# Performance work log

Measured on AMD Instinct MI355X. Metric: run time of the kernel, lower is better.

The kernel has to match this reference:

```python
import jax, jax.numpy as jnp
import numpy as np

EMBED_DIM = 1024
NUM_HEADS = 16
HEAD_DIM = EMBED_DIM // NUM_HEADS


def setup_inputs() -> dict:
    key = jax.random.key(0)
    ks = jax.random.split(key, 7)
    B, S, D = 8, 1024, EMBED_DIM
    scale = 1.0 / np.sqrt(D)
    x = jax.random.normal(ks[0], (B, S, D), dtype=jnp.float32)
    Wq = jax.random.normal(ks[1], (D, D), dtype=jnp.float32) * scale
    Wk = jax.random.normal(ks[2], (D, D), dtype=jnp.float32) * scale
    Wv = jax.random.normal(ks[3], (D, D), dtype=jnp.float32) * scale
    bq = jax.random.normal(ks[4], (D,), dtype=jnp.float32) * 0.01
    bk = jax.random.normal(ks[5], (D,), dtype=jnp.float32) * 0.01
    bv = jax.random.normal(ks[6], (D,), dtype=jnp.float32) * 0.01
    return {"x": x, "Wq": Wq, "Wk": Wk, "Wv": Wv, "bq": bq, "bk": bk, "bv": bv}


def reference(x, Wq, Wk, Wv, bq, bk, bv):
    B, S, D = x.shape
    H, Hd = NUM_HEADS, HEAD_DIM
    # torch nn.Linear: y = x @ W.T + b
    q = (x @ Wq.T + bq).reshape(B, S, H, Hd).transpose(0, 2, 1, 3)  # [B,H,S,Hd]
    k = (x @ Wk.T + bk).reshape(B, S, H, Hd).transpose(0, 2, 1, 3)
    v = (x @ Wv.T + bv).reshape(B, S, H, Hd).transpose(0, 2, 1, 3)
    scale = Hd ** -0.5
    scores = jnp.einsum('bhqd,bhkd->bhqk', q, k) * scale  # [B,H,S,S]
    attn = jax.nn.softmax(scores, axis=-1)
    # dropout_rate = 0.0 -> identity; out_proj is never applied in the source forward
    ctx = jnp.einsum('bhqk,bhkd->bhqd', attn, v)  # [B,H,S,Hd]
    return ctx.transpose(0, 2, 1, 3).reshape(B, S, D)
```

## Files before the change

kernel.cpp:

```cpp
#include <hip/hip_runtime.h>
#include <hip/hip_bf16.h>
#include <cstdint>
#include <cstddef>


typedef __attribute__((ext_vector_type(8))) short bf16x8;
typedef __attribute__((ext_vector_type(8))) unsigned short u16x8;
typedef __attribute__((ext_vector_type(4))) float f32x4;
typedef __attribute__((ext_vector_type(16))) float f32x16;
typedef __attribute__((ext_vector_type(4))) unsigned int u32x4;
typedef __attribute__((ext_vector_type(2))) unsigned int u32x2;

typedef const __attribute__((address_space(1))) void* gptr_t;
typedef __attribute__((address_space(3))) void* lptr_t;

#define LOG2E 1.44269504088896340736f

__device__ __forceinline__ unsigned short f2bf(float f) {
  unsigned int u = __float_as_uint(f);
  u += 0x7fffu + ((u >> 16) & 1u);
  return (unsigned short)(u >> 16);
}

__device__ __forceinline__ unsigned int pack_bf16x2(float lo, float hi) {
  const __hip_bfloat162 h = __float22bfloat162_rn(float2{lo, hi});
  unsigned int u;
  __builtin_memcpy(&u, &h, 4);
  return u;
}

__global__ void cvt_all(const float* __restrict__ x, const float* __restrict__ wq,
                        const float* __restrict__ wk, const float* __restrict__ wv,
                        unsigned short* __restrict__ Xb, unsigned short* __restrict__ Wb) {
  const int b = blockIdx.x;
  const float* src;
  unsigned short* dst;
  int i;
  if (b < 8192) {
    src = x; dst = Xb; i = b * 256 + threadIdx.x;
  } else {
    const int s = b - 8192;
    const int sel = s >> 10;
    src = (sel == 0) ? wq : (sel == 1) ? wk : wv;
    dst = Wb + (size_t)sel * 1048576;
    i = (s & 1023) * 256 + threadIdx.x;
  }
  float4 v = reinterpret_cast<const float4*>(src)[i];
  ushort4 o;
  o.x = f2bf(v.x); o.y = f2bf(v.y); o.z = f2bf(v.z); o.w = f2bf(v.w);
  reinterpret_cast<ushort4*>(dst)[i] = o;
}

__global__ __launch_bounds__(256) void qkv_gemm(
    const unsigned short* __restrict__ Xb, const unsigned short* __restrict__ Wb,
    const float* __restrict__ bq, const float* __restrict__ bk,
    const float* __restrict__ bv,
    unsigned short* __restrict__ Qo, unsigned short* __restrict__ Ko,
    unsigned short* __restrict__ Vo) {
  __shared__ unsigned short As[128 * 32];
  __shared__ unsigned short Bs[128 * 32];

  const int tid = threadIdx.x;
  const int lane = tid & 63;
  const int w = tid >> 6;
  const int wr = w >> 1, wc = w & 1;
  const int bm = blockIdx.x & 63;
  const int bn = blockIdx.x >> 6;

  const f32x4 vzero = {0.f, 0.f, 0.f, 0.f};
  f32x4 acc[4][4];
#pragma unroll
  for (int m = 0; m < 4; ++m)
#pragma unroll
    for (int n = 0; n < 4; ++n) acc[m][n] = vzero;

  const int c0 = w * 2, c1 = w * 2 + 1;
  const int srow0 = c0 * 16 + (lane >> 2);
  const int srow1 = c1 * 16 + (lane >> 2);
  const int scol = (lane & 3) * 8;
  const unsigned short* gA0 = Xb + (size_t)(bm * 128 + srow0) * 1024 + scol;
  const unsigned short* gA1 = Xb + (size_t)(bm * 128 + srow1) * 1024 + scol;
  const unsigned short* gB0 = Wb + (size_t)(bn * 128 + srow0) * 1024 + scol;
  const unsigned short* gB1 = Wb + (size_t)(bn * 128 + srow1) * 1024 + scol;
  char* lA0 = (char*)As + c0 * 1024;
  char* lA1 = (char*)As + c1 * 1024;
  char* lB0 = (char*)Bs + c0 * 1024;
  char* lB1 = (char*)Bs + c1 * 1024;

  const int aoff = (wr * 64 + (lane & 15)) * 64 + (lane >> 4) * 16;
  const int boff = (wc * 64 + (lane & 15)) * 64 + (lane >> 4) * 16;

  for (int kt = 0; kt < 32; ++kt) {
    const int k0 = kt * 32;
    __builtin_amdgcn_global_load_lds((gptr_t)(gA0 + k0), (lptr_t)lA0, 16, 0, 0);
    __builtin_amdgcn_global_load_lds((gptr_t)(gA1 + k0), (lptr_t)lA1, 16, 0, 0);
    __builtin_amdgcn_global_load_lds((gptr_t)(gB0 + k0), (lptr_t)lB0, 16, 0, 0);
    __builtin_amdgcn_global_load_lds((gptr_t)(gB1 + k0), (lptr_t)lB1, 16, 0, 0);
    __syncthreads();

    bf16x8 a[4], b[4];
#pragma unroll
    for (int m = 0; m < 4; ++m)
      a[m] = *reinterpret_cast<const bf16x8*>((const char*)As + aoff + m * 16 * 64);
#pragma unroll
    for (int n = 0; n < 4; ++n)
      b[n] = *reinterpret_cast<const bf16x8*>((const char*)Bs + boff + n * 16 * 64);
#pragma unroll
    for (int m = 0; m < 4; ++m)
#pragma unroll
      for (int n = 0; n < 4; ++n)
        acc[m][n] = __builtin_amdgcn_mfma_f32_16x16x32_bf16(a[m], b[n], acc[m][n], 0, 0, 0);
    __syncthreads();
  }

  const int t = bn >> 3;
  const float* bias = (t == 0) ? bq : (t == 1) ? bk : bv;
  unsigned short* dst = (t == 0) ? Qo : (t == 1) ? Ko : Vo;
  const float sc = (t == 0) ? 0.125f : 1.0f;
#pragma unroll
  for (int n = 0; n < 4; ++n) {
    const int gn = bn * 128 + wc * 64 + n * 16 + (lane & 15);
    const int d = gn & 1023;
    const int h = d >> 6, hd = d & 63;
    const float bias_v = bias[d];
#pragma unroll
    for (int m = 0; m < 4; ++m) {
      const int gm0 = bm * 128 + wr * 64 + m * 16 + ((lane >> 4) << 2);
      const int bb = gm0 >> 10;
      const int s0 = gm0 & 1023;
#pragma unroll
      for (int r = 0; r < 4; ++r) {
        dst[(((size_t)bb * 16 + h) * 1024 + (size_t)(s0 + r)) * 64 + hd] =
            f2bf((acc[m][n][r] + bias_v) * sc);
      }
    }
  }
}

__global__ __launch_bounds__(256) void transpose_v(
    const unsigned short* __restrict__ Vn, unsigned short* __restrict__ Vt) {
  __shared__ __align__(16) unsigned short T[64][72];
  const int tid = threadIdx.x;
  const int head = blockIdx.x & 127;
  const int st = blockIdx.x >> 7;
  const unsigned short* src = Vn + (size_t)head * 65536 + (size_t)st * 64 * 64;
  unsigned short* dst = Vt + (size_t)head * 65536 + (size_t)st * 64;
#pragma unroll
  for (int i = 0; i < 2; ++i) {
    const int idx = tid + i * 256;
    const int r = idx >> 3, ch = idx & 7;
    u16x8 v = *reinterpret_cast<const u16x8*>(src + r * 64 + ch * 8);
#pragma unroll
    for (int j = 0; j < 8; ++j)
      T[ch * 8 + j][r ^ (ch << 3)] = (unsigned short)v[j];
  }
  __syncthreads();
#pragma unroll
  for (int i = 0; i < 2; ++i) {
    const int idx = tid + i * 256;
    const int d = idx >> 3, ch = idx & 7;
    u16x8 v = *reinterpret_cast<const u16x8*>(&T[d][(ch ^ (d >> 3)) << 3]);
    *reinterpret_cast<u16x8*>(dst + (size_t)d * 1024 + ch * 8) = v;
  }
}

__global__ __launch_bounds__(512, 4) void attn32(
    const unsigned short* __restrict__ Q, const unsigned short* __restrict__ K,
    const unsigned short* __restrict__ Vt, float* __restrict__ out) {
  __shared__ __align__(16) char smem[3][16384];

  const int tid = threadIdx.x;
  const int lane = tid & 63;
  const int ln31 = lane & 31;
  const int g = lane >> 5;
  const int w = tid >> 6;
  const int head = blockIdx.x & 127;
  const int qt = blockIdx.x >> 7;

  const unsigned short* Qh = Q + (size_t)head * 65536;
  const unsigned short* Kh = K + (size_t)head * 65536;
  const unsigned short* Vh = Vt + (size_t)head * 65536;

  const int qrow = qt * 256 + w * 32 + ln31;
  bf16x8 qf[4];
#pragma unroll
  for (int dc = 0; dc < 4; ++dc)
    qf[dc] = *reinterpret_cast<const bf16x8*>(Qh + (size_t)qrow * 64 + dc * 16 + g * 8);
  asm volatile("s_waitcnt vmcnt(0)" ::: "memory");

  const int lb = w * 1024 + lane * 16;
  const int r = lb >> 7;
  const int c = ((((lb >> 4) & 7) ^ (r & 7)) << 3);
  const unsigned short* gK = Kh + r * 64 + c;
  const unsigned short* gV = Vh + r * 1024 + c;

#pragma unroll
  for (int pt = 0; pt < 2; ++pt) {
    char* b0 = smem[pt] + w * 1024;
    __builtin_amdgcn_global_load_lds((gptr_t)(gK + pt * 4096), (lptr_t)b0, 16, 0, 0);
    __builtin_amdgcn_global_load_lds((gptr_t)(gV + pt * 64), (lptr_t)(b0 + 8192), 16, 0, 0);
  }

  float l_ = 0.f;
  f32x16 acc0, acc1, z16;
#pragma unroll
  for (int i = 0; i < 16; ++i) { acc0[i] = 0.f; acc1[i] = 0.f; z16[i] = 0.f; }

  const int swz = (ln31 & 7) << 4;
  const int rowb0 = ln31 * 128;
  int boff[4];
#pragma unroll
  for (int dc = 0; dc < 4; ++dc) boff[dc] = ((((dc << 1) | g) << 4) ^ swz);

  const float MNL = 12.0f * LOG2E;

  for (int kt = 0; kt < 16; ++kt) {
    if (kt < 15) {
      asm volatile("s_waitcnt vmcnt(2)" ::: "memory");
    } else {
      asm volatile("s_waitcnt vmcnt(0)" ::: "memory");
    }
    __builtin_amdgcn_s_barrier();
    __builtin_amdgcn_sched_barrier(0);

    if (kt < 14) {
      char* nb = smem[(kt + 2) % 3] + w * 1024;
      __builtin_amdgcn_global_load_lds((gptr_t)(gK + (kt + 2) * 4096), (lptr_t)nb, 16, 0, 0);
      __builtin_amdgcn_global_load_lds((gptr_t)(gV + (kt + 2) * 64), (lptr_t)(nb + 8192), 16, 0, 0);
    }

    const char* Kb_ = smem[kt % 3] + rowb0;
    const char* Vb_ = Kb_ + 8192;

    f32x16 s0, s1;
    __builtin_amdgcn_s_setprio(1);
    {
      bf16x8 kf0 = *reinterpret_cast<const bf16x8*>(Kb_ + boff[0]);
      bf16x8 kf1 = *reinterpret_cast<const bf16x8*>(Kb_ + 4096 + boff[0]);
      s0 = __builtin_amdgcn_mfma_f32_32x32x16_bf16(kf0, qf[0], z16, 0, 0, 0);
      s1 = __builtin_amdgcn_mfma_f32_32x32x16_bf16(kf1, qf[0], z16, 0, 0, 0);
    }
#pragma unroll
    for (int dc = 1; dc < 4; ++dc) {
      bf16x8 kf0 = *reinterpret_cast<const bf16x8*>(Kb_ + boff[dc]);
      bf16x8 kf1 = *reinterpret_cast<const bf16x8*>(Kb_ + 4096 + boff[dc]);
      s0 = __builtin_amdgcn_mfma_f32_32x32x16_bf16(kf0, qf[dc], s0, 0, 0, 0);
      s1 = __builtin_amdgcn_mfma_f32_32x32x16_bf16(kf1, qf[dc], s1, 0, 0, 0);
    }
    __builtin_amdgcn_s_setprio(0);

    float ts = 0.f;
    unsigned int c_[8][2];
#pragma unroll
    for (int b = 0; b < 4; ++b) {
      const float p0 = exp2f(fmaf(s0[4 * b + 0], LOG2E, -MNL));
      const float p1 = exp2f(fmaf(s0[4 * b + 1], LOG2E, -MNL));
      const float p2 = exp2f(fmaf(s0[4 * b + 2], LOG2E, -MNL));
      const float p3 = exp2f(fmaf(s0[4 * b + 3], LOG2E, -MNL));
      ts += (p0 + p1) + (p2 + p3);
      c_[b][0] = pack_bf16x2(p0, p1);
      c_[b][1] = pack_bf16x2(p2, p3);
    }
#pragma unroll
    for (int b = 4; b < 8; ++b) {
      const float p0 = exp2f(fmaf(s1[4 * (b - 4) + 0], LOG2E, -MNL));
      const float p1 = exp2f(fmaf(s1[4 * (b - 4) + 1], LOG2E, -MNL));
      const float p2 = exp2f(fmaf(s1[4 * (b - 4) + 2], LOG2E, -MNL));
      const float p3 = exp2f(fmaf(s1[4 * (b - 4) + 3], LOG2E, -MNL));
      ts += (p0 + p1) + (p2 + p3);
      c_[b][0] = pack_bf16x2(p0, p1);
      c_[b][1] = pack_bf16x2(p2, p3);
    }
    {
      u32x2 rs = __builtin_amdgcn_permlane32_swap(
          __float_as_uint(ts), __float_as_uint(ts), false, false);
      ts = __uint_as_float(rs[0]) + __uint_as_float(rs[1]);
    }
    l_ += ts;

    __builtin_amdgcn_s_setprio(1);
#pragma unroll
    for (int t = 0; t < 4; ++t) {
      u32x4 pv;
#pragma unroll
      for (int i = 0; i < 2; ++i) {
        u32x2 rr = __builtin_amdgcn_permlane32_swap(
            c_[2 * t][i], c_[2 * t + 1][i], false, false);
        pv[i] = rr[0];
        pv[i + 2] = rr[1];
      }
      const bf16x8 pfv = __builtin_bit_cast(bf16x8, pv);
      bf16x8 vf0 = *reinterpret_cast<const bf16x8*>(Vb_ + boff[t]);
      bf16x8 vf1 = *reinterpret_cast<const bf16x8*>(Vb_ + 4096 + boff[t]);
      acc0 = __builtin_amdgcn_mfma_f32_32x32x16_bf16(vf0, pfv, acc0, 0, 0, 0);
      acc1 = __builtin_amdgcn_mfma_f32_32x32x16_bf16(vf1, pfv, acc1, 0, 0, 0);
    }
    __builtin_amdgcn_s_setprio(0);
  }

  const float invl = 1.0f / l_;
  const int bb = head >> 4, hh = head & 15;
  float* orow = out + ((size_t)bb * 1024 + qrow) * 1024 + hh * 64;
#pragma unroll
  for (int rq = 0; rq < 4; ++rq) {
    const int d0 = rq * 8 + g * 4;
    float4 v0, v1;
    v0.x = acc0[rq * 4 + 0] * invl; v0.y = acc0[rq * 4 + 1] * invl;
    v0.z = acc0[rq * 4 + 2] * invl; v0.w = acc0[rq * 4 + 3] * invl;
    v1.x = acc1[rq * 4 + 0] * invl; v1.y = acc1[rq * 4 + 1] * invl;
    v1.z = acc1[rq * 4 + 2] * invl; v1.w = acc1[rq * 4 + 3] * invl;
    *reinterpret_cast<float4*>(orow + d0) = v0;
    *reinterpret_cast<float4*>(orow + 32 + d0) = v1;
  }
}

extern "C" void kernel_launch(void* const* d_in, const int* in_sizes, int n_in,
                              void* d_out, int out_size, void* d_ws, size_t ws_size,
                              hipStream_t stream) {
  const float* x  = (const float*)d_in[0];
  const float* Wq = (const float*)d_in[1];
  const float* Wk = (const float*)d_in[2];
  const float* Wv = (const float*)d_in[3];
  const float* bq = (const float*)d_in[4];
  const float* bk = (const float*)d_in[5];
  const float* bv = (const float*)d_in[6];
  float* out = (float*)d_out;

  char* ws = (char*)d_ws;
  unsigned short* Xb = (unsigned short*)(ws);
  unsigned short* Wb = (unsigned short*)(ws + (size_t)16 * 1024 * 1024);
  unsigned short* Qb = (unsigned short*)(ws + (size_t)22 * 1024 * 1024);
  unsigned short* Kb = Qb + (size_t)8 * 1024 * 1024;
  unsigned short* Vb = Kb + (size_t)8 * 1024 * 1024;
  unsigned short* Vt = Xb;

  cvt_all<<<11264, 256, 0, stream>>>(x, Wq, Wk, Wv, Xb, Wb);

  qkv_gemm<<<1536, 256, 0, stream>>>(Xb, Wb, bq, bk, bv, Qb, Kb, Vb);

  transpose_v<<<2048, 256, 0, stream>>>(Vb, Vt);

  attn32<<<512, 512, 0, stream>>>(Qb, Kb, Vt, out);
}
```

Baseline: 142.2 us.

## Triple-buffer QKV GEMM LDS tiles with async prefetch and swizzled block order

The QKV projection GEMM now uses a three-stage LDS ring filled by global_load_lds, with two k-tiles prefetched ahead. Each step waits with a partial vmcnt and uses a single barrier per iteration instead of two. This overlaps global loads with MFMA work, and setprio raises wave priority during the MFMA block. Block indices are also remapped across groups of 8, likely to spread tiles across XCDs for better L2 reuse. LDS use grows to 48KB per block, which may lower occupancy.

Result: slower. 154.1 us (+8.4%).

```diff
diff --git a/kernel.cpp b/kernel.cpp
--- a/kernel.cpp
+++ b/kernel.cpp
@@ -57,15 +57,15 @@
     const float* __restrict__ bv,
     unsigned short* __restrict__ Qo, unsigned short* __restrict__ Ko,
     unsigned short* __restrict__ Vo) {
-  __shared__ unsigned short As[128 * 32];
-  __shared__ unsigned short Bs[128 * 32];
+  __shared__ __align__(16) char smem[3][16384];
 
   const int tid = threadIdx.x;
   const int lane = tid & 63;
   const int w = tid >> 6;
   const int wr = w >> 1, wc = w & 1;
-  const int bm = blockIdx.x & 63;
-  const int bn = blockIdx.x >> 6;
+  const int sbid = (blockIdx.x & 7) * 192 + (blockIdx.x >> 3);
+  const int bm = sbid & 63;
+  const int bn = sbid >> 6;
 
   const f32x4 vzero = {0.f, 0.f, 0.f, 0.f};
   f32x4 acc[4][4];
@@ -82,35 +82,57 @@
   const unsigned short* gA1 = Xb + (size_t)(bm * 128 + srow1) * 1024 + scol;
   const unsigned short* gB0 = Wb + (size_t)(bn * 128 + srow0) * 1024 + scol;
   const unsigned short* gB1 = Wb + (size_t)(bn * 128 + srow1) * 1024 + scol;
-  char* lA0 = (char*)As + c0 * 1024;
-  char* lA1 = (char*)As + c1 * 1024;
-  char* lB0 = (char*)Bs + c0 * 1024;
-  char* lB1 = (char*)Bs + c1 * 1024;
+  const int lA0o = c0 * 1024;
+  const int lA1o = c1 * 1024;
+  const int lB0o = 8192 + c0 * 1024;
+  const int lB1o = 8192 + c1 * 1024;
 
   const int aoff = (wr * 64 + (lane & 15)) * 64 + (lane >> 4) * 16;
-  const int boff = (wc * 64 + (lane & 15)) * 64 + (lane >> 4) * 16;
+  const int boff = 8192 + (wc * 64 + (lane & 15)) * 64 + (lane >> 4) * 16;
+
+#pragma unroll
+  for (int pt = 0; pt < 2; ++pt) {
+    char* bb_ = smem[pt];
+    const int k0 = pt * 32;
+    __builtin_amdgcn_global_load_lds((gptr_t)(gA0 + k0), (lptr_t)(bb_ + lA0o), 16, 0, 0);
+    __builtin_amdgcn_global_load_lds((gptr_t)(gA1 + k0), (lptr_t)(bb_ + lA1o), 16, 0, 0);
+    __builtin_amdgcn_global_load_lds((gptr_t)(gB0 + k0), (lptr_t)(bb_ + lB0o), 16, 0, 0);
+    __builtin_amdgcn_global_load_lds((gptr_t)(gB1 + k0), (lptr_t)(bb_ + lB1o), 16, 0, 0);
+  }
 
   for (int kt = 0; kt < 32; ++kt) {
-    const int k0 = kt * 32;
-    __builtin_amdgcn_global_load_lds((gptr_t)(gA0 + k0), (lptr_t)lA0, 16, 0, 0);
-    __builtin_amdgcn_global_load_lds((gptr_t)(gA1 + k0), (lptr_t)lA1, 16, 0, 0);
-    __builtin_amdgcn_global_load_lds((gptr_t)(gB0 + k0), (lptr_t)lB0, 16, 0, 0);
-    __builtin_amdgcn_global_load_lds((gptr_t)(gB1 + k0), (lptr_t)lB1, 16, 0, 0);
-    __syncthreads();
-
+    if (kt < 31) {
+      asm volatile("s_waitcnt vmcnt(4)" ::: "memory");
+    } else {
+      asm volatile("s_waitcnt vmcnt(0)" ::: "memory");
+    }
+    __builtin_amdgcn_s_barrier();
+    __builtin_amdgcn_sched_barrier(0);
+
+    if (kt < 30) {
+      char* nb = smem[(kt + 2) % 3];
+      const int k0 = (kt + 2) * 32;
+      __builtin_amdgcn_global_load_lds((gptr_t)(gA0 + k0), (lptr_t)(nb + lA0o), 16, 0, 0);
+      __builtin_amdgcn_global_load_lds((gptr_t)(gA1 + k0), (lptr_t)(nb + lA1o), 16, 0, 0);
+      __builtin_amdgcn_global_load_lds((gptr_t)(gB0 + k0), (lptr_t)(nb + lB0o), 16, 0, 0);
+      __builtin_amdgcn_global_load_lds((gptr_t)(gB1 + k0), (lptr_t)(nb + lB1o), 16, 0, 0);
+    }
+
+    const char* buf = smem[kt % 3];
     bf16x8 a[4], b[4];
 #pragma unroll
     for (int m = 0; m < 4; ++m)
-      a[m] = *reinterpret_cast<const bf16x8*>((const char*)As + aoff + m * 16 * 64);
+      a[m] = *reinterpret_cast<const bf16x8*>(buf + aoff + m * 16 * 64);
 #pragma unroll
     for (int n = 0; n < 4; ++n)
-      b[n] = *reinterpret_cast<const bf16x8*>((const char*)Bs + boff + n * 16 * 64);
+      b[n] = *reinterpret_cast<const bf16x8*>(buf + boff + n * 16 * 64);
+    __builtin_amdgcn_s_setprio(1);
 #pragma unroll
     for (int m = 0; m < 4; ++m)
 #pragma unroll
       for (int n = 0; n < 4; ++n)
         acc[m][n] = __builtin_amdgcn_mfma_f32_16x16x32_bf16(a[m], b[n], acc[m][n], 0, 0, 0);
-    __syncthreads();
+    __builtin_amdgcn_s_setprio(0);
   }
 
   const int t = bn >> 3;
```
